# Optimization experiments

Hardware: AMD Instinct MI355X
Metric: run time of the kernel (lower is better)

## Reference

```python
import jax, jax.numpy as jnp
import numpy as np

INPUT_DIM = 1024
OUTPUT_DIM = 1024
DOWN = INPUT_DIM // 8  # reduction_factor=8
NUM_TOKENS = 2


def setup_inputs() -> dict:
    key = jax.random.key(0)
    k1, k2, k3, k4, k5 = jax.random.split(key, 5)
    B, Sx, Sy = 32, 2048, 512
    x = jax.random.normal(k1, (B, Sx, INPUT_DIM), dtype=jnp.float32)
    y = jax.random.normal(k2, (B, Sy, INPUT_DIM), dtype=jnp.float32)
    # nn.Parameter(torch.rand(...)) -> uniform [0,1)
    latent_tokens = jax.random.uniform(k3, (NUM_TOKENS, INPUT_DIM), dtype=jnp.float32)
    gate = jnp.zeros((1,), dtype=jnp.float32)
    # Conv1d kernel_size=1, no bias == pointwise matmul; kaiming-uniform-ish init
    lim_d = 1.0 / np.sqrt(INPUT_DIM)
    lim_u = 1.0 / np.sqrt(DOWN)
    W_down = jax.random.uniform(k4, (DOWN, INPUT_DIM), dtype=jnp.float32, minval=-lim_d, maxval=lim_d)
    W_up = jax.random.uniform(k5, (OUTPUT_DIM, DOWN), dtype=jnp.float32, minval=-lim_u, maxval=lim_u)
    return {"x": x, "y": y, "latent_tokens": latent_tokens, "gate": gate,
            "W_down": W_down, "W_up": W_up}


def reference(x, y, latent_tokens, gate, W_down, W_up):
    # tokens attend over y:  [B,T,Sy] softmax over Sy
    att_y2t = jax.nn.softmax(jnp.einsum('td,bsd->bts', latent_tokens, y), axis=-1)
    tokens = latent_tokens[None] + jnp.einsum('bts,bsd->btd', att_y2t, y)  # [B,T,D]
    # x attends over tokens: [B,Sx,T] softmax over T
    att_t2x = jax.nn.softmax(jnp.einsum('bsd,btd->bst', x, tokens), axis=-1)
    x_res = jnp.einsum('bst,btd->bsd', att_t2x, tokens)
    x = x + gate * x_res
    # 1x1 conv bottleneck: down -> ReLU -> up (pointwise matmuls)
    z = jax.nn.relu(jnp.einsum('bsd,ed->bse', x, W_down))
    out = jnp.einsum('bse,oe->bso', z, W_up)
    return out
```

## Files before the change

### kernel.cpp

```cpp
#include <hip/hip_runtime.h>
#include <hip/hip_bf16.h>

#define B_N 32
#define SX 2048
#define SY 512
#define DIM 1024
#define NTOK 2
#define DN 128
#define ODIM 1024
#define BM 64
#define BK 64
#define NT 16
#define RING 4

typedef __bf16 bf16;
typedef __bf16 bf16x8 __attribute__((ext_vector_type(8)));
typedef __bf16 bf16x4 __attribute__((ext_vector_type(4)));
typedef float f32x4 __attribute__((ext_vector_type(4)));

typedef __attribute__((address_space(3))) unsigned char lds_u8;
typedef const __attribute__((address_space(1))) unsigned char glb_u8;

__device__ __forceinline__ f32x4 mfma16(bf16x8 a, bf16x8 b, f32x4 c) {
  return __builtin_amdgcn_mfma_f32_16x16x32_bf16(a, b, c, 0, 0, 0);
}
__device__ __forceinline__ void gll16(const void* g, void* l) {
  __builtin_amdgcn_global_load_lds((glb_u8*)g, (lds_u8*)l, 16, 0, 0);
}

__global__ __launch_bounds__(256) void prep_kernel(const float* __restrict__ Wd,
                                                   const float* __restrict__ Wu,
                                                   bf16* __restrict__ wdb,
                                                   bf16* __restrict__ wub) {
  int i = blockIdx.x * 256 + threadIdx.x;
  if (i < DN * DIM) {
    wdb[i] = (bf16)Wd[i];
    wub[i] = (bf16)Wu[i];
  }
}

__global__ __launch_bounds__(256) void tokens_kernel(const float* __restrict__ y,
                                                     const float* __restrict__ lat,
                                                     const float* __restrict__ gate,
                                                     float* __restrict__ tokens) {
  if (gate[0] == 0.0f) return;
  __shared__ float s_lat[NTOK][DIM];
  __shared__ float s_sc[NTOK][SY];
  int b = blockIdx.x;
  int tid = threadIdx.x, wave = tid >> 6, lane = tid & 63;
  const float* yb = y + (size_t)b * SY * DIM;
  for (int i = tid; i < NTOK * DIM; i += 256) ((float*)s_lat)[i] = lat[i];
  __syncthreads();
  for (int s = wave * 128; s < wave * 128 + 128; ++s) {
    const float* yr = yb + (size_t)s * DIM;
    float d0 = 0.f, d1 = 0.f;
#pragma unroll
    for (int i = 0; i < 4; ++i) {
      f32x4 v = *(const f32x4*)(yr + lane * 4 + i * 256);
      f32x4 l0 = *(const f32x4*)(&s_lat[0][lane * 4 + i * 256]);
      f32x4 l1 = *(const f32x4*)(&s_lat[1][lane * 4 + i * 256]);
      d0 += v[0] * l0[0] + v[1] * l0[1] + v[2] * l0[2] + v[3] * l0[3];
      d1 += v[0] * l1[0] + v[1] * l1[1] + v[2] * l1[2] + v[3] * l1[3];
    }
#pragma unroll
    for (int off = 32; off > 0; off >>= 1) {
      d0 += __shfl_xor(d0, off);
      d1 += __shfl_xor(d1, off);
    }
    if (lane == 0) { s_sc[0][s] = d0; s_sc[1][s] = d1; }
  }
  __syncthreads();
  if (wave < 2) {
    float m = -3.4e38f;
    for (int s = lane; s < SY; s += 64) m = fmaxf(m, s_sc[wave][s]);
#pragma unroll
    for (int off = 32; off > 0; off >>= 1) m = fmaxf(m, __shfl_xor(m, off));
    float sum = 0.f;
    for (int s = lane; s < SY; s += 64) {
      float e = expf(s_sc[wave][s] - m);
      s_sc[wave][s] = e;
      sum += e;
    }
#pragma unroll
    for (int off = 32; off > 0; off >>= 1) sum += __shfl_xor(sum, off);
    float inv = 1.f / sum;
    for (int s = lane; s < SY; s += 64) s_sc[wave][s] *= inv;
  }
  __syncthreads();
  float a0[4] = {0.f, 0.f, 0.f, 0.f}, a1[4] = {0.f, 0.f, 0.f, 0.f};
  for (int s = 0; s < SY; ++s) {
    float p0 = s_sc[0][s], p1 = s_sc[1][s];
    const float* yr = yb + (size_t)s * DIM;
#pragma unroll
    for (int i = 0; i < 4; ++i) {
      float v = yr[tid + i * 256];
      a0[i] += p0 * v;
      a1[i] += p1 * v;
    }
  }
  float* tb = tokens + (size_t)b * NTOK * DIM;
#pragma unroll
  for (int i = 0; i < 4; ++i) {
    tb[tid + i * 256] = s_lat[0][tid + i * 256] + a0[i];
    tb[DIM + tid + i * 256] = s_lat[1][tid + i * 256] + a1[i];
  }
}

__global__ __launch_bounds__(256) void xprime_kernel(const float* __restrict__ x,
                                                     const float* __restrict__ gate,
                                                     const float* __restrict__ tokens,
                                                     float* __restrict__ xp) {
  float g = gate[0];
  if (g == 0.0f) return;
  __shared__ float s_tok[NTOK][DIM];
  __shared__ float s_c[BM][2];
  int tid = threadIdx.x, w = tid >> 6, lane = tid & 63;
  size_t m0 = (size_t)blockIdx.x * BM;
  int b = (int)(m0 / SX);
  const float* xb = x + m0 * DIM;
  const float* tokb = tokens + (size_t)b * NTOK * DIM;
  for (int i = tid; i < NTOK * DIM; i += 256) ((float*)s_tok)[i] = tokb[i];
  __syncthreads();
  for (int i = 0; i < 16; ++i) {
    int r = w * 16 + i;
    const float* xrow = xb + (size_t)r * DIM;
    float d0 = 0.f, d1 = 0.f;
#pragma unroll
    for (int c = 0; c < 4; ++c) {
      f32x4 v = *(const f32x4*)(xrow + lane * 4 + c * 256);
      f32x4 t0 = *(const f32x4*)(&s_tok[0][lane * 4 + c * 256]);
      f32x4 t1 = *(const f32x4*)(&s_tok[1][lane * 4 + c * 256]);
      d0 += v[0] * t0[0] + v[1] * t0[1] + v[2] * t0[2] + v[3] * t0[3];
      d1 += v[0] * t1[0] + v[1] * t1[1] + v[2] * t1[2] + v[3] * t1[3];
    }
#pragma unroll
    for (int off = 32; off > 0; off >>= 1) {
      d0 += __shfl_xor(d0, off);
      d1 += __shfl_xor(d1, off);
    }
    if (lane == 0) {
      float mm = fmaxf(d0, d1);
      float e0 = expf(d0 - mm), e1 = expf(d1 - mm);
      float inv = g / (e0 + e1);
      s_c[r][0] = e0 * inv;
      s_c[r][1] = e1 * inv;
    }
  }
  __syncthreads();
  float* xpb = xp + m0 * DIM;
  for (int r = w * 16; r < w * 16 + 16; ++r) {
    float c0 = s_c[r][0], c1 = s_c[r][1];
#pragma unroll
    for (int c = 0; c < 4; ++c) {
      f32x4 v = *(const f32x4*)(xb + (size_t)r * DIM + lane * 4 + c * 256);
      f32x4 t0 = *(const f32x4*)(&s_tok[0][lane * 4 + c * 256]);
      f32x4 t1 = *(const f32x4*)(&s_tok[1][lane * 4 + c * 256]);
      f32x4 o;
#pragma unroll
      for (int j = 0; j < 4; ++j) o[j] = v[j] + c0 * t0[j] + c1 * t1[j];
      *(f32x4*)(xpb + (size_t)r * DIM + lane * 4 + c * 256) = o;
    }
  }
}

__global__ __launch_bounds__(512) void main_kernel(const float* __restrict__ x,
                                                   const float* __restrict__ gate,
                                                   const float* __restrict__ xp,
                                                   const bf16* __restrict__ wdb,
                                                   const bf16* __restrict__ wub,
                                                   float* __restrict__ out) {
  __shared__ __align__(16) char smem[147456];

  int tid = threadIdx.x, w = tid >> 6, l = tid & 63;
  int lq = l >> 4, lr = l & 15;
  int wr = w >> 2, wc = w & 3;
  size_t m0 = (size_t)blockIdx.x * BM;
  float g = gate[0];
  const float* xb = ((g != 0.f) ? xp : x) + m0 * DIM;

  const char* xsrc[2];
  const char* wsrc[2];
#pragma unroll
  for (int j = 0; j < 2; ++j) {
    int xr = w * 8 + j * 4 + (l >> 4);
    int xcb = ((l & 15) * 16) ^ ((j * 4 + (l >> 4)) << 5);
    xsrc[j] = (const char*)xb + (size_t)xr * (DIM * 4) + xcb;
    int wr_ = w * 16 + j * 8 + (l >> 3);
    int wcb = ((l & 7) * 16) ^ ((l >> 3) << 4);
    wsrc[j] = (const char*)wdb + (size_t)wr_ * (DIM * 2) + wcb;
  }

  f32x4 acc[2][2] = {};

  auto STAGE = [&](int t) {
    int b = t & 3;
#pragma unroll
    for (int j = 0; j < 2; ++j)
      gll16(xsrc[j] + (size_t)t * (BK * 4),
            smem + b * 16384 + (w * 8 + j * 4) * 256);
#pragma unroll
    for (int j = 0; j < 2; ++j)
      gll16(wsrc[j] + (size_t)t * (BK * 2),
            smem + 65536 + b * 16384 + (w * 16 + j * 8) * 128);
  };

  auto COMP = [&](int b) {
    const char* xt = smem + b * 16384;
    const char* wt = smem + 65536 + b * 16384;
    __builtin_amdgcn_s_setprio(1);
#pragma unroll
    for (int kc = 0; kc < 2; ++kc) {
      bf16x8 wdf[2];
#pragma unroll
      for (int nf = 0; nf < 2; ++nf) {
        int dn = wc * 32 + nf * 16 + lr;
        wdf[nf] = *(const bf16x8*)(wt + dn * 128 +
                                   ((kc * 64 + lq * 16) ^ ((lr & 7) << 4)));
      }
#pragma unroll
      for (int mt = 0; mt < 2; ++mt) {
        int row = wr * 32 + mt * 16 + lr;
        int sz = (row & 7) << 5;
        int kb = kc * 128 + lq * 32;
        f32x4 a0 = *(const f32x4*)(xt + row * 256 + (kb ^ sz));
        f32x4 a1 = *(const f32x4*)(xt + row * 256 + ((kb + 16) ^ sz));
        bf16x8 xf;
#pragma unroll
        for (int jj = 0; jj < 4; ++jj) {
          xf[jj] = (bf16)a0[jj];
          xf[4 + jj] = (bf16)a1[jj];
        }
        acc[mt][0] = mfma16(wdf[0], xf, acc[mt][0]);
        acc[mt][1] = mfma16(wdf[1], xf, acc[mt][1]);
      }
    }
    __builtin_amdgcn_s_setprio(0);
  };

  STAGE(0);
  STAGE(1);
  STAGE(2);
  STAGE(3);

#pragma unroll
  for (int t = 0; t < NT; ++t) {
    if (t <= NT - 4) {
      asm volatile("s_waitcnt vmcnt(12)" ::: "memory");
    } else if (t == NT - 3) {
      asm volatile("s_waitcnt vmcnt(8)" ::: "memory");
    } else if (t == NT - 2) {
      asm volatile("s_waitcnt vmcnt(4)" ::: "memory");
    } else {
      asm volatile("s_waitcnt vmcnt(0)" ::: "memory");
    }
    __builtin_amdgcn_sched_barrier(0);
    __builtin_amdgcn_s_barrier();
    COMP(t & 3);
    __builtin_amdgcn_sched_barrier(0);
    __builtin_amdgcn_s_barrier();
    if (t + 4 < NT) STAGE(t + 4);
  }

  char* zls = smem + 131072;
#pragma unroll
  for (int mt = 0; mt < 2; ++mt)
#pragma unroll
    for (int nf = 0; nf < 2; ++nf) {
      int xr = wr * 32 + mt * 16 + lr;
      int dn = wc * 32 + nf * 16 + lq * 4;
      bf16x4 pk;
#pragma unroll
      for (int r = 0; r < 4; ++r) pk[r] = (bf16)fmaxf(acc[mt][nf][r], 0.f);
      *(bf16x4*)(zls + xr * (DN * 2) + ((dn * 2) ^ ((xr & 7) << 4))) = pk;
    }
  __syncthreads();

  bf16x8 zF[4][4];
#pragma unroll
  for (int mt = 0; mt < 4; ++mt)
#pragma unroll
    for (int kt = 0; kt < 4; ++kt) {
      int xr = mt * 16 + lr;
      zF[kt][mt] = *(const bf16x8*)(zls + xr * (DN * 2) +
                                    (((kt * 32 + lq * 8) * 2) ^ ((xr & 7) << 4)));
    }

  float* ob = out + m0 * ODIM;
#pragma unroll 2
  for (int oc16 = 0; oc16 < 8; ++oc16) {
    int base = w * 128 + oc16 * 16;
    bf16x8 wu[4];
#pragma unroll
    for (int kt = 0; kt < 4; ++kt)
      wu[kt] = *(const bf16x8*)(wub + (size_t)(base + lr) * DN + kt * 32 + lq * 8);
    f32x4 a2[4] = {};
#pragma unroll
    for (int kt = 0; kt < 4; ++kt)
#pragma unroll
      for (int mt = 0; mt < 4; ++mt)
        a2[mt] = mfma16(wu[kt], zF[kt][mt], a2[mt]);
#pragma unroll
    for (int mt = 0; mt < 4; ++mt)
      *(f32x4*)(ob + (size_t)(mt * 16 + lr) * ODIM + base + lq * 4) = a2[mt];
  }
}

extern "C" void kernel_launch(void* const* d_in, const int* in_sizes, int n_in,
                              void* d_out, int out_size, void* d_ws, size_t ws_size,
                              hipStream_t stream) {
  const float* x = (const float*)d_in[0];
  const float* y = (const float*)d_in[1];
  const float* lat = (const float*)d_in[2];
  const float* gate = (const float*)d_in[3];
  const float* Wd = (const float*)d_in[4];
  const float* Wu = (const float*)d_in[5];
  float* out = (float*)d_out;
  char* ws = (char*)d_ws;

  float* tokens = (float*)ws;
  bf16* wdb = (bf16*)(ws + 262144);
  bf16* wub = (bf16*)(ws + 524288);

  prep_kernel<<<(DN * DIM + 255) / 256, 256, 0, stream>>>(Wd, Wu, wdb, wub);
  tokens_kernel<<<B_N, 256, 0, stream>>>(y, lat, gate, tokens);
  xprime_kernel<<<(B_N * SX) / BM, 256, 0, stream>>>(x, gate, tokens, out);
  main_kernel<<<(B_N * SX) / BM, 512, 0, stream>>>(x, gate, out, wdb, wub, out);
}
```

Measured before the change: 144.8 us.

## Process two row panels per block, overlapping up-projection epilogue with next panel's GEMM

Each block now handles two 64-row panels. The first panel's up-projection epilogue and output stores are interleaved with the second panel's down-projection K loop, so MFMA and store work overlap with the global-to-LDS loads. W_up fragments are hoisted into registers once per block and reused for both panels. This halves the grid and raises register pressure with the 8x4 bf16x8 W_up array, which may cut occupancy or cause spills, and the vmcnt bookkeeping has to account for the extra outstanding loads.

```diff
diff --git a/kernel.cpp b/kernel.cpp
--- a/kernel.cpp
+++ b/kernel.cpp
@@ -11,7 +11,6 @@
 #define BM 64
 #define BK 64
 #define NT 16
-#define RING 4
 
 typedef __bf16 bf16;
 typedef __bf16 bf16x8 __attribute__((ext_vector_type(8)));
@@ -26,6 +25,16 @@
 }
 __device__ __forceinline__ void gll16(const void* g, void* l) {
   __builtin_amdgcn_global_load_lds((glb_u8*)g, (lds_u8*)l, 16, 0, 0);
+}
+__device__ __forceinline__ void waitv(int n) {
+  switch (n) {
+    case 0: asm volatile("s_waitcnt vmcnt(0)" ::: "memory"); break;
+    case 4: asm volatile("s_waitcnt vmcnt(4)" ::: "memory"); break;
+    case 8: asm volatile("s_waitcnt vmcnt(8)" ::: "memory"); break;
+    case 12: asm volatile("s_waitcnt vmcnt(12)" ::: "memory"); break;
+    case 16: asm volatile("s_waitcnt vmcnt(16)" ::: "memory"); break;
+    default: asm volatile("s_waitcnt vmcnt(20)" ::: "memory"); break;
+  }
 }
 
 __global__ __launch_bounds__(256) void prep_kernel(const float* __restrict__ Wd,
@@ -174,9 +183,17 @@
   int tid = threadIdx.x, w = tid >> 6, l = tid & 63;
   int lq = l >> 4, lr = l & 15;
   int wr = w >> 2, wc = w & 3;
-  size_t m0 = (size_t)blockIdx.x * BM;
+  size_t m0 = (size_t)blockIdx.x * (2 * BM);
   float g = gate[0];
-  const float* xb = ((g != 0.f) ? xp : x) + m0 * DIM;
+  const float* xbA = ((g != 0.f) ? xp : x) + m0 * DIM;
+
+  bf16x8 wu[8][4];
+#pragma unroll
+  for (int s = 0; s < 8; ++s)
+#pragma unroll
+    for (int kt = 0; kt < 4; ++kt)
+      wu[s][kt] = *(const bf16x8*)(wub + (size_t)(w * 128 + s * 16 + lr) * DN +
+                                   kt * 32 + lq * 8);
 
   const char* xsrc[2];
   const char* wsrc[2];
@@ -184,19 +201,20 @@
   for (int j = 0; j < 2; ++j) {
     int xr = w * 8 + j * 4 + (l >> 4);
     int xcb = ((l & 15) * 16) ^ ((j * 4 + (l >> 4)) << 5);
-    xsrc[j] = (const char*)xb + (size_t)xr * (DIM * 4) + xcb;
+    xsrc[j] = (const char*)xbA + (size_t)xr * (DIM * 4) + xcb;
     int wr_ = w * 16 + j * 8 + (l >> 3);
     int wcb = ((l & 7) * 16) ^ ((l >> 3) << 4);
     wsrc[j] = (const char*)wdb + (size_t)wr_ * (DIM * 2) + wcb;
   }
+  const size_t POFF = (size_t)BM * DIM * 4;
 
   f32x4 acc[2][2] = {};
 
-  auto STAGE = [&](int t) {
+  auto STAGE = [&](int t, int panel) {
     int b = t & 3;
 #pragma unroll
     for (int j = 0; j < 2; ++j)
-      gll16(xsrc[j] + (size_t)t * (BK * 4),
+      gll16(xsrc[j] + (size_t)panel * POFF + (size_t)t * (BK * 4),
             smem + b * 16384 + (w * 8 + j * 4) * 256);
 #pragma unroll
     for (int j = 0; j < 2; ++j)
@@ -237,72 +255,97 @@
     __builtin_amdgcn_s_setprio(0);
   };
 
-  STAGE(0);
-  STAGE(1);
-  STAGE(2);
-  STAGE(3);
-
+  auto ZWRITE = [&]() {
+    char* zls = smem + 131072;
+#pragma unroll
+    for (int mt = 0; mt < 2; ++mt)
+#pragma unroll
+      for (int nf = 0; nf < 2; ++nf) {
+        int xr = wr * 32 + mt * 16 + lr;
+        int dn = wc * 32 + nf * 16 + lq * 4;
+        bf16x4 pk;
+#pragma unroll
+        for (int r = 0; r < 4; ++r) pk[r] = (bf16)fmaxf(acc[mt][nf][r], 0.f);
+        *(bf16x4*)(zls + xr * (DN * 2) + ((dn * 2) ^ ((xr & 7) << 4))) = pk;
+      }
+  };
+
+  auto EPI = [&](int s, const bf16x8(&zF)[4][4], float* ob) {
+    f32x4 a2[4] = {};
+#pragma unroll
+    for (int kt = 0; kt < 4; ++kt)
+#pragma unroll
+      for (int mt = 0; mt < 4; ++mt)
+        a2[mt] = mfma16(wu[s][kt], zF[kt][mt], a2[mt]);
+#pragma unroll
+    for (int mt = 0; mt < 4; ++mt)
+      *(f32x4*)(ob + (size_t)(mt * 16 + lr) * ODIM + w * 128 + s * 16 + lq * 4) = a2[mt];
+  };
+
+  char* zls = smem + 131072;
+
+  STAGE(0, 0); STAGE(1, 0); STAGE(2, 0); STAGE(3, 0);
 #pragma unroll
   for (int t = 0; t < NT; ++t) {
-    if (t <= NT - 4) {
-      asm volatile("s_waitcnt vmcnt(12)" ::: "memory");
-    } else if (t == NT - 3) {
-      asm volatile("s_waitcnt vmcnt(8)" ::: "memory");
-    } else if (t == NT - 2) {
-      asm volatile("s_waitcnt vmcnt(4)" ::: "memory");
-    } else {
-      asm volatile("s_waitcnt vmcnt(0)" ::: "memory");
-    }
+    waitv(t <= NT - 4 ? 12 : (t == NT - 3 ? 8 : (t == NT - 2 ? 4 : 0)));
     __builtin_amdgcn_sched_barrier(0);
     __builtin_amdgcn_s_barrier();
     COMP(t & 3);
     __builtin_amdgcn_sched_barrier(0);
     __builtin_amdgcn_s_barrier();
-    if (t + 4 < NT) STAGE(t + 4);
-  }
-
-  char* zls = smem + 131072;
-#pragma unroll
-  for (int mt = 0; mt < 2; ++mt)
-#pragma unroll
-    for (int nf = 0; nf < 2; ++nf) {
-      int xr = wr * 32 + mt * 16 + lr;
-      int dn = wc * 32 + nf * 16 + lq * 4;
-      bf16x4 pk;
-#pragma unroll
-      for (int r = 0; r < 4; ++r) pk[r] = (bf16)fmaxf(acc[mt][nf][r], 0.f);
-      *(bf16x4*)(zls + xr * (DN * 2) + ((dn * 2) ^ ((xr & 7) << 4))) = pk;
-    }
-  __syncthreads();
-
-  bf16x8 zF[4][4];
+    if (t + 4 < NT) STAGE(t + 4, 0);
+  }
+
+  STAGE(0, 1); STAGE(1, 1); STAGE(2, 1); STAGE(3, 1);
+  ZWRITE();
+  asm volatile("s_waitcnt lgkmcnt(0)" ::: "memory");
+  __builtin_amdgcn_sched_barrier(0);
+  __builtin_amdgcn_s_barrier();
+  bf16x8 zFA[4][4];
 #pragma unroll
   for (int mt = 0; mt < 4; ++mt)
 #pragma unroll
     for (int kt = 0; kt < 4; ++kt) {
       int xr = mt * 16 + lr;
-      zF[kt][mt] = *(const bf16x8*)(zls + xr * (DN * 2) +
-                                    (((kt * 32 + lq * 8) * 2) ^ ((xr & 7) << 4)));
-    }
-
-  float* ob = out + m0 * ODIM;
-#pragma unroll 2
-  for (int oc16 = 0; oc16 < 8; ++oc16) {
-    int base = w * 128 + oc16 * 16;
-    bf16x8 wu[4];
-#pragma unroll
-    for (int kt = 0; kt < 4; ++kt)
-      wu[kt] = *(const bf16x8*)(wub + (size_t)(base + lr) * DN + kt * 32 + lq * 8);
-    f32x4 a2[4] = {};
-#pragma unroll
-    for (int kt = 0; kt < 4; ++kt)
-#pragma unroll
-      for (int mt = 0; mt < 4; ++mt)
-        a2[mt] = mfma16(wu[kt], zF[kt][mt], a2[mt]);
-#pragma unroll
-    for (int mt = 0; mt < 4; ++mt)
-      *(f32x4*)(ob + (size_t)(mt * 16 + lr) * ODIM + base + lq * 4) = a2[mt];
-  }
+      zFA[kt][mt] = *(const bf16x8*)(zls + xr * (DN * 2) +
+                                     (((kt * 32 + lq * 8) * 2) ^ ((xr & 7) << 4)));
+    }
+#pragma unroll
+  for (int mt = 0; mt < 2; ++mt)
+#pragma unroll
+    for (int nf = 0; nf < 2; ++nf) acc[mt][nf] = (f32x4){0.f, 0.f, 0.f, 0.f};
+
+  float* obA = out + m0 * ODIM;
+  constexpr int WB[16] = {12, 16, 16, 20, 20, 20, 20, 20,
+                          20, 20, 20, 20, 20, 16, 12, 8};
+#pragma unroll
+  for (int t = 0; t < NT; ++t) {
+    waitv(WB[t]);
+    __builtin_amdgcn_sched_barrier(0);
+    __builtin_amdgcn_s_barrier();
+    COMP(t & 3);
+    __builtin_amdgcn_sched_barrier(0);
+    __builtin_amdgcn_s_barrier();
+    if (t + 4 < NT) STAGE(t + 4, 1);
+    if ((t & 1) == 0) EPI(t >> 1, zFA, obA);
+  }
+
+  ZWRITE();
+  asm volatile("s_waitcnt lgkmcnt(0)" ::: "memory");
+  __builtin_amdgcn_sched_barrier(0);
+  __builtin_amdgcn_s_barrier();
+  bf16x8 zFB[4][4];
+#pragma unroll
+  for (int mt = 0; mt < 4; ++mt)
+#pragma unroll
+    for (int kt = 0; kt < 4; ++kt) {
+      int xr = mt * 16 + lr;
+      zFB[kt][mt] = *(const bf16x8*)(zls + xr * (DN * 2) +
+                                     (((kt * 32 + lq * 8) * 2) ^ ((xr & 7) << 4)));
+    }
+  float* obB = out + (m0 + BM) * ODIM;
+#pragma unroll
+  for (int s = 0; s < 8; ++s) EPI(s, zFB, obB);
 }
 
 extern "C" void kernel_launch(void* const* d_in, const int* in_sizes, int n_in,
@@ -324,5 +367,5 @@
   prep_kernel<<<(DN * DIM + 255) / 256, 256, 0, stream>>>(Wd, Wu, wdb, wub);
   tokens_kernel<<<B_N, 256, 0, stream>>>(y, lat, gate, tokens);
   xprime_kernel<<<(B_N * SX) / BM, 256, 0, stream>>>(x, gate, tokens, out);
-  main_kernel<<<(B_N * SX) / BM, 512, 0, stream>>>(x, gate, out, wdb, wub, out);
-}
+  main_kernel<<<(B_N * SX) / (2 * BM), 512, 0, stream>>>(x, gate, out, wdb, wub, out);
+}
```

New measurement: 183.1 us. 1.27x slower.
